# Performance work log

Measured on AMD Instinct MI355X. Metric: run time of the kernel, lower is better.

## Reference

```python
import jax, jax.numpy as jnp
import numpy as np

B, T, C, H = 32, 256, 512, 512
T_OUT = 8 * T  # fixed padded expanded length (max duration per token = 8)
ALPHA = 1.0
EPS = 1e-5


def _layer_norm(x, g, b):
    mu = jnp.mean(x, axis=-1, keepdims=True)
    var = jnp.mean(jnp.square(x - mu), axis=-1, keepdims=True)
    return (x - mu) * jax.lax.rsqrt(var + EPS) * g + b


def _conv1d_same(x, w, b):
    # x: [B,T,Cin], w: [3,Cin,Cout] -> [B,T,Cout]
    y = jax.lax.conv_general_dilated(x, w, window_strides=(1,), padding='SAME',
                                     dimension_numbers=('NWC', 'WIO', 'NWC'))
    return y + b


def setup_inputs() -> dict:
    key = jax.random.key(0)
    ks = jax.random.split(key, 8)
    s1 = 1.0 / np.sqrt(3 * C)
    s2 = 1.0 / np.sqrt(3 * H)
    return {
        'x': jax.random.normal(ks[0], (B, T, C), jnp.float32),
        'true_durations': jax.random.randint(ks[1], (B, T), 0, 8, jnp.int32),
        'W1': jax.random.normal(ks[2], (3, C, H), jnp.float32) * s1,
        'b1': jnp.zeros((H,), jnp.float32),
        'g1': jnp.ones((H,), jnp.float32),
        'beta1': jnp.zeros((H,), jnp.float32),
        'W2': jax.random.normal(ks[3], (3, H, H), jnp.float32) * s2,
        'b2': jnp.zeros((H,), jnp.float32),
        'g2': jnp.ones((H,), jnp.float32),
        'beta2': jnp.zeros((H,), jnp.float32),
        'Wl': jax.random.normal(ks[4], (H, 1), jnp.float32) * (1.0 / np.sqrt(H)),
        'bl': jnp.zeros((1,), jnp.float32),
    }


def _duration_predictor(x, W1, b1, g1, beta1, W2, b2, g2, beta2, Wl, bl):
    h = jax.nn.relu(_layer_norm(_conv1d_same(x, W1, b1), g1, beta1))
    h = jax.nn.relu(_layer_norm(_conv1d_same(h, W2, b2), g2, beta2))
    return (h @ Wl + bl)[..., 0]  # [B,T]


def _expand_by_durations(x, dur):
    # cumsum-based gather: output position t takes source token i where
    # csum[i-1] <= t < csum[i]; positions >= total length are zero-padded.
    csum = jnp.cumsum(dur, axis=-1)  # [B,T]
    pos = jnp.arange(T_OUT, dtype=csum.dtype)  # [T_OUT]
    idx = jax.vmap(lambda c: jnp.searchsorted(c, pos, side='right'))(csum)  # [B,T_OUT]
    valid = pos[None, :] < csum[:, -1:]
    idx = jnp.clip(idx, 0, dur.shape[1] - 1)
    out = jnp.take_along_axis(x, idx[..., None], axis=1)  # [B,T_OUT,C]
    return out * valid[..., None].astype(x.dtype)


def reference(x, true_durations, W1, b1, g1, beta1, W2, b2, g2, beta2, Wl, bl):
    log_lengths = _duration_predictor(x, W1, b1, g1, beta1, W2, b2, g2, beta2, Wl, bl) * ALPHA
    res = _expand_by_durations(x, true_durations)
    return res, log_lengths
```

## Files before the change

### kernel.cpp

```cpp
#include <hip/hip_runtime.h>
#include <hip/hip_bf16.h>

#define B_    32
#define T_    256
#define C_    512
#define H_    512
#define TOUT_ 2048
#define TP_   258
#define K_    1536
#define EPS_  1e-5f

typedef __attribute__((ext_vector_type(8))) short bf16x8;
typedef __attribute__((ext_vector_type(4))) float f32x4;

#define GLL16(g, l)                                                        \
  __builtin_amdgcn_global_load_lds(                                        \
      (const __attribute__((address_space(1))) void*)(g),                  \
      (__attribute__((address_space(3))) void*)(l), 16, 0, 0)

__device__ __forceinline__ void wt_convert_block(const float* __restrict__ W,
                                                 __hip_bfloat16* __restrict__ Wt,
                                                 int k0, int n0, int tid,
                                                 float* tile ) {
  const int tx = tid & 31;
  const int ty = tid >> 5;
#pragma unroll
  for (int i = 0; i < 4; ++i)
    tile[(ty * 4 + i) * 33 + tx] = W[(size_t)(k0 + ty * 4 + i) * H_ + n0 + tx];
  __syncthreads();
#pragma unroll
  for (int i = 0; i < 4; ++i)
    Wt[(size_t)(n0 + ty * 4 + i) * K_ + k0 + tx] =
        __float2bfloat16(tile[tx * 33 + ty * 4 + i]);
}

__device__ __forceinline__ void csum_block(const int* __restrict__ dur,
                                           int* __restrict__ csum,
                                           int b, int tid, int* wsum) {
  int v = dur[b * T_ + tid];
#pragma unroll
  for (int off = 1; off < 64; off <<= 1) {
    int u = __shfl_up(v, off);
    if ((tid & 63) >= off) v += u;
  }
  if ((tid & 63) == 63) wsum[tid >> 6] = v;
  __syncthreads();
  int base = 0;
#pragma unroll
  for (int j = 0; j < 4; ++j)
    if (j < (tid >> 6)) base += wsum[j];
  csum[b * T_ + tid] = v + base;
}

__device__ __forceinline__ void expand_copy_block(const float* __restrict__ X,
                                                  const int* __restrict__ csum,
                                                  float* __restrict__ res,
                                                  int u, int tid) {
  const int wave = (tid >> 6) & 3, lane = tid & 63;
#pragma unroll
  for (int k = 0; k < 4; ++k) {
    const int sr = u * 16 + wave * 4 + k;
    const int b = sr >> 8, t = sr & 255;
    const int* cb = csum + b * T_;
    const int c0 = t ? cb[t - 1] : 0;
    const int d  = cb[t] - c0;
    if (d == 0) continue;
    const float* src = X + (size_t)sr * C_;
    const float4 v0 = *(const float4*)(src + lane * 4);
    const float4 v1 = *(const float4*)(src + 256 + lane * 4);
    float* dst = res + ((size_t)b * TOUT_ + c0) * C_;
    for (int j = 0; j < d; ++j) {
      *(float4*)(dst + (size_t)j * C_ + lane * 4)       = v0;
      *(float4*)(dst + (size_t)j * C_ + 256 + lane * 4) = v1;
    }
  }
}

__device__ __forceinline__ void expand_zero_block(const int* __restrict__ csum,
                                                  float* __restrict__ res,
                                                  int z, int tid) {
  const int b  = z >> 6;
  const int t0 = (z & 63) << 5;
  const int total = csum[b * T_ + 255];
  const float4 z4 = make_float4(0.f, 0.f, 0.f, 0.f);
  const int half = (tid >> 7) & 1, c4 = tid & 127;
#pragma unroll
  for (int rr = half; rr < 32; rr += 2) {
    const int r = t0 + rr;
    if (r >= total)
      *(float4*)(res + ((size_t)b * TOUT_ + r) * C_ + c4 * 4) = z4;
  }
}

__global__ __launch_bounds__(256) void prep_kernel(const float* __restrict__ X,
                                                   const float* __restrict__ W1,
                                                   const int* __restrict__ dur,
                                                   __hip_bfloat16* __restrict__ xpad,
                                                   __hip_bfloat16* __restrict__ hpad,
                                                   __hip_bfloat16* __restrict__ Wt1,
                                                   int* __restrict__ csum) {
  __shared__ float tile[32 * 33];
  const int tid = threadIdx.x;
  if (blockIdx.x >= 4896) {
    csum_block(dur, csum, blockIdx.x - 4896, tid, (int*)tile);
    return;
  }
  if (blockIdx.x >= 4128) {
    const int id = blockIdx.x - 4128;
    wt_convert_block(W1, Wt1, (id % 48) * 32, (id / 48) * 32, tid, tile);
    return;
  }
  const int row = blockIdx.x * 2 + (tid >> 7);
  const int b = row / TP_;
  const int t = row - b * TP_;
  const int c = (tid & 127) * 4;
  __hip_bfloat16* dst = xpad + (size_t)row * C_ + c;
  if (t == 0 || t == TP_ - 1) {
    ushort4 zz = make_ushort4(0, 0, 0, 0);
    *(ushort4*)dst = zz;
    *(ushort4*)(hpad + (size_t)row * C_ + c) = zz;
    return;
  }
  const float4 v = *(const float4*)(X + (size_t)(b * T_ + t - 1) * C_ + c);
  union { __hip_bfloat16 h[4]; ushort4 u; } o;
  o.h[0] = __float2bfloat16(v.x);
  o.h[1] = __float2bfloat16(v.y);
  o.h[2] = __float2bfloat16(v.z);
  o.h[3] = __float2bfloat16(v.w);
  *(ushort4*)dst = o.u;
}

__global__ __launch_bounds__(512) void conv_expand_kernel(
    const __hip_bfloat16* __restrict__ Apad,
    const __hip_bfloat16* __restrict__ Wt,
    const float* __restrict__ bias,
    float* __restrict__ Y,
    const float* __restrict__ X,
    const int* __restrict__ csum,
    float* __restrict__ res,
    const float* __restrict__ W2,
    __hip_bfloat16* __restrict__ Wt2,
    int ex_base) {
  __shared__ __hip_bfloat16 smA[2][2][4096];
  __shared__ __hip_bfloat16 smB[2][2][4096];

  const int tid = threadIdx.x;

  if (blockIdx.x >= 896) {
    const int id = (blockIdx.x - 896) * 2 + (tid >> 8);
    float* tile = (float*)smA + (tid >> 8) * (32 * 33);
    wt_convert_block(W2, Wt2, (id % 48) * 32, (id / 48) * 32, tid & 255, tile);
    return;
  }
  if (blockIdx.x >= 256) {
    const int u = ex_base + (blockIdx.x - 256) * 2 + (tid >> 8);
    const int st = tid & 255;
    if (u < 512) expand_copy_block(X, csum, res, u, st);
    else         expand_zero_block(csum, res, u - 512, st);
    return;
  }

  const int lane = tid & 63;
  const int wid  = tid >> 6;
  const int cid  = blockIdx.x;
  const int n0 = (cid & 3) << 7;
  const int m0 = (cid >> 2) << 7;
  const int b  = m0 >> 8;
  const int t0 = m0 & 255;
  const int wm = (wid >> 2) << 6;
  const int wn = (wid & 3) << 5;

  const int rowS = tid >> 2;
  const int gsw  = ((tid & 3) + rowS) & 3;
  const __hip_bfloat16* arowA = Apad + (size_t)(b * TP_ + t0 + rowS) * C_ + (gsw << 3);
  const __hip_bfloat16* browB = Wt + (size_t)(n0 + rowS) * K_ + (gsw << 3);

  f32x4 acc[4][2] = {};

  auto stage = [&](int buf, int k0) {
    const int kw = k0 >> 9;
    const int c0 = k0 & 511;
    const __hip_bfloat16* a0 = arowA + kw * C_ + c0;
    GLL16(a0,           &smA[buf][0][tid << 3]);
    GLL16(a0 + 32,      &smA[buf][1][tid << 3]);
    GLL16(browB + k0,      &smB[buf][0][tid << 3]);
    GLL16(browB + k0 + 32, &smB[buf][1][tid << 3]);
  };

  auto compute = [&](int buf) {
    const int g   = lane >> 4;
    const int r15 = lane & 15;
    const int sa  = ((g - r15) & 3) << 3;
#pragma unroll
    for (int sl = 0; sl < 2; ++sl) {
      const __hip_bfloat16* As = smA[buf][sl];
      const __hip_bfloat16* Bs = smB[buf][sl];
      bf16x8 aF[4], bF[2];
#pragma unroll
      for (int i = 0; i < 4; ++i)
        aF[i] = *(const bf16x8*)(As + ((wm + (i << 4) + r15) << 5) + sa);
#pragma unroll
      for (int i = 0; i < 2; ++i)
        bF[i] = *(const bf16x8*)(Bs + ((wn + (i << 4) + r15) << 5) + sa);
#pragma unroll
      for (int mi = 0; mi < 4; ++mi)
#pragma unroll
        for (int ni = 0; ni < 2; ++ni)
          acc[mi][ni] = __builtin_amdgcn_mfma_f32_16x16x32_bf16(
              aF[mi], bF[ni], acc[mi][ni], 0, 0, 0);
    }
  };

  asm volatile("s_waitcnt vmcnt(0)" ::: "memory");
  stage(0, 0);
  stage(1, 64);

  for (int s = 0; s < 22; ++s) {
    asm volatile("s_waitcnt vmcnt(4)" ::: "memory");
    __builtin_amdgcn_sched_barrier(0);
    __builtin_amdgcn_s_barrier();
    compute(s & 1);
    asm volatile("s_waitcnt lgkmcnt(0)" ::: "memory");
    __builtin_amdgcn_s_barrier();
    stage(s & 1, (s + 2) << 6);
  }
  asm volatile("s_waitcnt vmcnt(4)" ::: "memory");
  __builtin_amdgcn_sched_barrier(0);
  __builtin_amdgcn_s_barrier();
  compute(0);
  asm volatile("s_waitcnt vmcnt(0)" ::: "memory");
  __builtin_amdgcn_sched_barrier(0);
  __builtin_amdgcn_s_barrier();
  compute(1);

  const int cn_base = n0 + wn + (lane & 15);
  const int rm_base = m0 + wm + ((lane >> 4) << 2);
#pragma unroll
  for (int ni = 0; ni < 2; ++ni) {
    const int cn = cn_base + (ni << 4);
    const float bb = bias[cn];
#pragma unroll
    for (int mi = 0; mi < 4; ++mi) {
#pragma unroll
      for (int rq = 0; rq < 4; ++rq) {
        const int rm = rm_base + (mi << 4) + rq;
        Y[(size_t)rm * H_ + cn] = acc[mi][ni][rq] + bb;
      }
    }
  }
}

__global__ __launch_bounds__(256) void ln_relu_pad_kernel(const float* __restrict__ in,
                                                          const float* __restrict__ g,
                                                          const float* __restrict__ beta,
                                                          __hip_bfloat16* __restrict__ outpad) {
  const int wave = threadIdx.x >> 6;
  const int lane = threadIdx.x & 63;
  const int row  = blockIdx.x * 4 + wave;
  const float* r = in + (size_t)row * H_;

  const float4 v0 = *(const float4*)(r + lane * 4);
  const float4 v1 = *(const float4*)(r + 256 + lane * 4);

  float s = v0.x + v0.y + v0.z + v0.w + v1.x + v1.y + v1.z + v1.w;
  float q = v0.x * v0.x + v0.y * v0.y + v0.z * v0.z + v0.w * v0.w +
            v1.x * v1.x + v1.y * v1.y + v1.z * v1.z + v1.w * v1.w;
#pragma unroll
  for (int off = 32; off; off >>= 1) {
    s += __shfl_xor(s, off);
    q += __shfl_xor(q, off);
  }
  const float mu  = s * (1.0f / 512.0f);
  const float var = q * (1.0f / 512.0f) - mu * mu;
  const float rs  = rsqrtf(var + EPS_);

  const float4 g0 = *(const float4*)(g + lane * 4);
  const float4 g1 = *(const float4*)(g + 256 + lane * 4);
  const float4 e0 = *(const float4*)(beta + lane * 4);
  const float4 e1 = *(const float4*)(beta + 256 + lane * 4);

  union { __hip_bfloat16 h[4]; ushort4 u; } o0, o1;
  o0.h[0] = __float2bfloat16(fmaxf(0.f, (v0.x - mu) * rs * g0.x + e0.x));
  o0.h[1] = __float2bfloat16(fmaxf(0.f, (v0.y - mu) * rs * g0.y + e0.y));
  o0.h[2] = __float2bfloat16(fmaxf(0.f, (v0.z - mu) * rs * g0.z + e0.z));
  o0.h[3] = __float2bfloat16(fmaxf(0.f, (v0.w - mu) * rs * g0.w + e0.w));
  o1.h[0] = __float2bfloat16(fmaxf(0.f, (v1.x - mu) * rs * g1.x + e1.x));
  o1.h[1] = __float2bfloat16(fmaxf(0.f, (v1.y - mu) * rs * g1.y + e1.y));
  o1.h[2] = __float2bfloat16(fmaxf(0.f, (v1.z - mu) * rs * g1.z + e1.z));
  o1.h[3] = __float2bfloat16(fmaxf(0.f, (v1.w - mu) * rs * g1.w + e1.w));

  const int bq = row >> 8, t = row & 255;
  __hip_bfloat16* w = outpad + (size_t)(bq * TP_ + t + 1) * H_;
  *(ushort4*)(w + lane * 4)       = o0.u;
  *(ushort4*)(w + 256 + lane * 4) = o1.u;
}

__global__ __launch_bounds__(256) void ln_relu_linear_kernel(const float* __restrict__ in,
                                                             const float* __restrict__ g,
                                                             const float* __restrict__ beta,
                                                             const float* __restrict__ Wl,
                                                             const float* __restrict__ bl,
                                                             float* __restrict__ out) {
  const int wave = threadIdx.x >> 6;
  const int lane = threadIdx.x & 63;
  const int row  = blockIdx.x * 4 + wave;
  const float* r = in + (size_t)row * H_;

  const float4 v0 = *(const float4*)(r + lane * 4);
  const float4 v1 = *(const float4*)(r + 256 + lane * 4);

  float s = v0.x + v0.y + v0.z + v0.w + v1.x + v1.y + v1.z + v1.w;
  float q = v0.x * v0.x + v0.y * v0.y + v0.z * v0.z + v0.w * v0.w +
            v1.x * v1.x + v1.y * v1.y + v1.z * v1.z + v1.w * v1.w;
#pragma unroll
  for (int off = 32; off; off >>= 1) {
    s += __shfl_xor(s, off);
    q += __shfl_xor(q, off);
  }
  const float mu  = s * (1.0f / 512.0f);
  const float var = q * (1.0f / 512.0f) - mu * mu;
  const float rs  = rsqrtf(var + EPS_);

  const float4 g0 = *(const float4*)(g + lane * 4);
  const float4 g1 = *(const float4*)(g + 256 + lane * 4);
  const float4 e0 = *(const float4*)(beta + lane * 4);
  const float4 e1 = *(const float4*)(beta + 256 + lane * 4);
  const float4 w0 = *(const float4*)(Wl + lane * 4);
  const float4 w1 = *(const float4*)(Wl + 256 + lane * 4);

  float sd = 0.f;
  sd += fmaxf(0.f, (v0.x - mu) * rs * g0.x + e0.x) * w0.x;
  sd += fmaxf(0.f, (v0.y - mu) * rs * g0.y + e0.y) * w0.y;
  sd += fmaxf(0.f, (v0.z - mu) * rs * g0.z + e0.z) * w0.z;
  sd += fmaxf(0.f, (v0.w - mu) * rs * g0.w + e0.w) * w0.w;
  sd += fmaxf(0.f, (v1.x - mu) * rs * g1.x + e1.x) * w1.x;
  sd += fmaxf(0.f, (v1.y - mu) * rs * g1.y + e1.y) * w1.y;
  sd += fmaxf(0.f, (v1.z - mu) * rs * g1.z + e1.z) * w1.z;
  sd += fmaxf(0.f, (v1.w - mu) * rs * g1.w + e1.w) * w1.w;
#pragma unroll
  for (int off = 32; off; off >>= 1) sd += __shfl_xor(sd, off);

  if (lane == 0) out[row] = sd + bl[0];
}

extern "C" void kernel_launch(void* const* d_in, const int* in_sizes, int n_in,
                              void* d_out, int out_size, void* d_ws, size_t ws_size,
                              hipStream_t stream) {
  const float* x     = (const float*)d_in[0];
  const int*   dur   = (const int*)d_in[1];
  const float* W1    = (const float*)d_in[2];
  const float* b1    = (const float*)d_in[3];
  const float* g1    = (const float*)d_in[4];
  const float* beta1 = (const float*)d_in[5];
  const float* W2    = (const float*)d_in[6];
  const float* b2    = (const float*)d_in[7];
  const float* g2    = (const float*)d_in[8];
  const float* beta2 = (const float*)d_in[9];
  const float* Wl    = (const float*)d_in[10];
  const float* bl    = (const float*)d_in[11];

  float* out = (float*)d_out;
  float* res    = out;
  float* loglen = out + (size_t)B_ * TOUT_ * C_;

  char* ws = (char*)d_ws;
  __hip_bfloat16* xpad = (__hip_bfloat16*)ws;
  __hip_bfloat16* hpad = xpad + (size_t)B_ * TP_ * C_;
  __hip_bfloat16* Wt1  = hpad + (size_t)B_ * TP_ * C_;
  __hip_bfloat16* Wt2  = Wt1 + (size_t)H_ * K_;
  float* tmp1 = (float*)(Wt2 + (size_t)H_ * K_);
  int*   csum = (int*)(tmp1 + (size_t)B_ * T_ * H_);

  prep_kernel<<<4928, 256, 0, stream>>>(x, W1, dur, xpad, hpad, Wt1, csum);

  conv_expand_kernel<<<1280, 512, 0, stream>>>(xpad, Wt1, b1, tmp1,
                                               x, csum, res, W2, Wt2, 0);
  ln_relu_pad_kernel<<<B_ * T_ / 4, 256, 0, stream>>>(tmp1, g1, beta1, hpad);

  conv_expand_kernel<<<896, 512, 0, stream>>>(hpad, Wt2, b2, tmp1,
                                              x, csum, res, nullptr, nullptr, 1280);
  ln_relu_linear_kernel<<<B_ * T_ / 4, 256, 0, stream>>>(tmp1, g2, beta2, Wl, bl, loglen);
}
```

Measured before the change: 82.60 us.

## Fuse LayerNorm, ReLU and output projection into full-width conv GEMM epilogue

Each conv GEMM block now computes a full 128x512 output tile, so the whole hidden row is held in registers. That lets it apply bias, LayerNorm (via cross-wave partial sums in LDS), ReLU, and either the bf16 padded write or the final linear dot product directly in the epilogue. This removes the fp32 intermediate buffer round trips and the two standalone LayerNorm kernel launches. The trade-off is that only 64 GEMM blocks remain, each doing four times more work with a large accumulator footprint under a 2-blocks-per-CU bound. That raises the risk of register spills and of the GEMM becoming a long critical path next to the expand blocks.

```diff
diff --git a/kernel.cpp b/kernel.cpp
--- a/kernel.cpp
+++ b/kernel.cpp
@@ -130,30 +130,36 @@
   *(ushort4*)dst = o.u;
 }
 
-__global__ __launch_bounds__(512) void conv_expand_kernel(
+template <int MODE>
+__global__ __launch_bounds__(512, 2) void conv_fused_kernel(
     const __hip_bfloat16* __restrict__ Apad,
     const __hip_bfloat16* __restrict__ Wt,
     const float* __restrict__ bias,
-    float* __restrict__ Y,
+    const float* __restrict__ gam,
+    const float* __restrict__ bet,
+    const float* __restrict__ Wl,
+    const float* __restrict__ bl,
+    __hip_bfloat16* __restrict__ hout,
+    float* __restrict__ lout,
     const float* __restrict__ X,
     const int* __restrict__ csum,
     float* __restrict__ res,
     const float* __restrict__ W2,
     __hip_bfloat16* __restrict__ Wt2,
     int ex_base) {
-  __shared__ __hip_bfloat16 smA[2][2][4096];
-  __shared__ __hip_bfloat16 smB[2][2][4096];
+  __shared__ __hip_bfloat16 smA[2][4096];
+  __shared__ __hip_bfloat16 smB[2][16384];
 
   const int tid = threadIdx.x;
 
-  if (blockIdx.x >= 896) {
-    const int id = (blockIdx.x - 896) * 2 + (tid >> 8);
-    float* tile = (float*)smA + (tid >> 8) * (32 * 33);
+  if (blockIdx.x >= 704) {
+    const int id = (blockIdx.x - 704) * 2 + (tid >> 8);
+    float* tile = (float*)&smB[0][0] + (tid >> 8) * (32 * 33);
     wt_convert_block(W2, Wt2, (id % 48) * 32, (id / 48) * 32, tid & 255, tile);
     return;
   }
-  if (blockIdx.x >= 256) {
-    const int u = ex_base + (blockIdx.x - 256) * 2 + (tid >> 8);
+  if (blockIdx.x >= 64) {
+    const int u = ex_base + (blockIdx.x - 64) * 2 + (tid >> 8);
     const int st = tid & 255;
     if (u < 512) expand_copy_block(X, csum, res, u, st);
     else         expand_zero_block(csum, res, u - 512, st);
@@ -162,69 +168,64 @@
 
   const int lane = tid & 63;
   const int wid  = tid >> 6;
-  const int cid  = blockIdx.x;
-  const int n0 = (cid & 3) << 7;
-  const int m0 = (cid >> 2) << 7;
+  const int m0 = blockIdx.x << 7;
   const int b  = m0 >> 8;
   const int t0 = m0 & 255;
-  const int wm = (wid >> 2) << 6;
-  const int wn = (wid & 3) << 5;
+  const int wgrp   = wid >> 2;
+  const int wslice = wid & 3;
+  const int wm  = wgrp << 6;
+  const int wnn = wslice << 7;
 
   const int rowS = tid >> 2;
   const int gsw  = ((tid & 3) + rowS) & 3;
   const __hip_bfloat16* arowA = Apad + (size_t)(b * TP_ + t0 + rowS) * C_ + (gsw << 3);
-  const __hip_bfloat16* browB = Wt + (size_t)(n0 + rowS) * K_ + (gsw << 3);
-
-  f32x4 acc[4][2] = {};
+  const __hip_bfloat16* browB = Wt + (size_t)rowS * K_ + (gsw << 3);
+
+  f32x4 acc[4][8] = {};
 
   auto stage = [&](int buf, int k0) {
     const int kw = k0 >> 9;
     const int c0 = k0 & 511;
-    const __hip_bfloat16* a0 = arowA + kw * C_ + c0;
-    GLL16(a0,           &smA[buf][0][tid << 3]);
-    GLL16(a0 + 32,      &smA[buf][1][tid << 3]);
-    GLL16(browB + k0,      &smB[buf][0][tid << 3]);
-    GLL16(browB + k0 + 32, &smB[buf][1][tid << 3]);
+    GLL16(arowA + kw * C_ + c0, &smA[buf][tid << 3]);
+#pragma unroll
+    for (int j = 0; j < 4; ++j)
+      GLL16(browB + (size_t)(j * 128) * K_ + k0,
+            &smB[buf][(tid << 3) + (j << 12)]);
   };
 
   auto compute = [&](int buf) {
     const int g   = lane >> 4;
     const int r15 = lane & 15;
     const int sa  = ((g - r15) & 3) << 3;
-#pragma unroll
-    for (int sl = 0; sl < 2; ++sl) {
-      const __hip_bfloat16* As = smA[buf][sl];
-      const __hip_bfloat16* Bs = smB[buf][sl];
-      bf16x8 aF[4], bF[2];
-#pragma unroll
-      for (int i = 0; i < 4; ++i)
-        aF[i] = *(const bf16x8*)(As + ((wm + (i << 4) + r15) << 5) + sa);
-#pragma unroll
-      for (int i = 0; i < 2; ++i)
-        bF[i] = *(const bf16x8*)(Bs + ((wn + (i << 4) + r15) << 5) + sa);
-#pragma unroll
-      for (int mi = 0; mi < 4; ++mi)
-#pragma unroll
-        for (int ni = 0; ni < 2; ++ni)
-          acc[mi][ni] = __builtin_amdgcn_mfma_f32_16x16x32_bf16(
-              aF[mi], bF[ni], acc[mi][ni], 0, 0, 0);
-    }
+    bf16x8 aF[4], bF[8];
+#pragma unroll
+    for (int i = 0; i < 4; ++i)
+      aF[i] = *(const bf16x8*)(&smA[buf][((wm + (i << 4) + r15) << 5) + sa]);
+#pragma unroll
+    for (int i = 0; i < 8; ++i)
+      bF[i] = *(const bf16x8*)(&smB[buf][((wnn + (i << 4) + r15) << 5) + sa]);
+#pragma unroll
+    for (int mi = 0; mi < 4; ++mi)
+#pragma unroll
+      for (int ni = 0; ni < 8; ++ni)
+        acc[mi][ni] = __builtin_amdgcn_mfma_f32_16x16x32_bf16(
+            aF[mi], bF[ni], acc[mi][ni], 0, 0, 0);
   };
 
   asm volatile("s_waitcnt vmcnt(0)" ::: "memory");
   stage(0, 0);
-  stage(1, 64);
-
-  for (int s = 0; s < 22; ++s) {
-    asm volatile("s_waitcnt vmcnt(4)" ::: "memory");
+  stage(1, 32);
+
+  for (int s = 0; s < 46; ++s) {
+    asm volatile("s_waitcnt vmcnt(5)" ::: "memory");
     __builtin_amdgcn_sched_barrier(0);
     __builtin_amdgcn_s_barrier();
     compute(s & 1);
     asm volatile("s_waitcnt lgkmcnt(0)" ::: "memory");
     __builtin_amdgcn_s_barrier();
-    stage(s & 1, (s + 2) << 6);
-  }
-  asm volatile("s_waitcnt vmcnt(4)" ::: "memory");
+    stage(s & 1, (s + 2) << 5);
+  }
+  asm volatile("s_waitcnt vmcnt(5)" ::: "memory");
   __builtin_amdgcn_sched_barrier(0);
   __builtin_amdgcn_s_barrier();
   compute(0);
@@ -233,114 +234,103 @@
   __builtin_amdgcn_s_barrier();
   compute(1);
 
-  const int cn_base = n0 + wn + (lane & 15);
-  const int rm_base = m0 + wm + ((lane >> 4) << 2);
-#pragma unroll
-  for (int ni = 0; ni < 2; ++ni) {
-    const int cn = cn_base + (ni << 4);
-    const float bb = bias[cn];
-#pragma unroll
-    for (int mi = 0; mi < 4; ++mi) {
-#pragma unroll
-      for (int rq = 0; rq < 4; ++rq) {
-        const int rm = rm_base + (mi << 4) + rq;
-        Y[(size_t)rm * H_ + cn] = acc[mi][ni][rq] + bb;
+  __syncthreads();
+  float* scr  = (float*)&smA[0][0];
+  float* scr2 = scr + 2048;
+
+  const int g   = lane >> 4;
+  const int r15 = lane & 15;
+
+  float bb8[8];
+#pragma unroll
+  for (int ni = 0; ni < 8; ++ni) bb8[ni] = bias[wnn + (ni << 4) + r15];
+
+#pragma unroll
+  for (int mi = 0; mi < 4; ++mi)
+#pragma unroll
+    for (int rq = 0; rq < 4; ++rq) {
+      float s = 0.f, q = 0.f;
+#pragma unroll
+      for (int ni = 0; ni < 8; ++ni) {
+        const float v = acc[mi][ni][rq] + bb8[ni];
+        s += v; q += v * v;
+      }
+#pragma unroll
+      for (int off = 1; off < 16; off <<= 1) {
+        s += __shfl_xor(s, off);
+        q += __shfl_xor(q, off);
+      }
+      if (r15 == 0) {
+        const int lrow = (mi << 4) + (g << 2) + rq;
+        const int base = (((wgrp << 6) + lrow) << 3) + (wslice << 1);
+        scr[base]     = s;
+        scr[base + 1] = q;
       }
     }
-  }
-}
-
-__global__ __launch_bounds__(256) void ln_relu_pad_kernel(const float* __restrict__ in,
-                                                          const float* __restrict__ g,
-                                                          const float* __restrict__ beta,
-                                                          __hip_bfloat16* __restrict__ outpad) {
-  const int wave = threadIdx.x >> 6;
-  const int lane = threadIdx.x & 63;
-  const int row  = blockIdx.x * 4 + wave;
-  const float* r = in + (size_t)row * H_;
-
-  const float4 v0 = *(const float4*)(r + lane * 4);
-  const float4 v1 = *(const float4*)(r + 256 + lane * 4);
-
-  float s = v0.x + v0.y + v0.z + v0.w + v1.x + v1.y + v1.z + v1.w;
-  float q = v0.x * v0.x + v0.y * v0.y + v0.z * v0.z + v0.w * v0.w +
-            v1.x * v1.x + v1.y * v1.y + v1.z * v1.z + v1.w * v1.w;
-#pragma unroll
-  for (int off = 32; off; off >>= 1) {
-    s += __shfl_xor(s, off);
-    q += __shfl_xor(q, off);
-  }
-  const float mu  = s * (1.0f / 512.0f);
-  const float var = q * (1.0f / 512.0f) - mu * mu;
-  const float rs  = rsqrtf(var + EPS_);
-
-  const float4 g0 = *(const float4*)(g + lane * 4);
-  const float4 g1 = *(const float4*)(g + 256 + lane * 4);
-  const float4 e0 = *(const float4*)(beta + lane * 4);
-  const float4 e1 = *(const float4*)(beta + 256 + lane * 4);
-
-  union { __hip_bfloat16 h[4]; ushort4 u; } o0, o1;
-  o0.h[0] = __float2bfloat16(fmaxf(0.f, (v0.x - mu) * rs * g0.x + e0.x));
-  o0.h[1] = __float2bfloat16(fmaxf(0.f, (v0.y - mu) * rs * g0.y + e0.y));
-  o0.h[2] = __float2bfloat16(fmaxf(0.f, (v0.z - mu) * rs * g0.z + e0.z));
-  o0.h[3] = __float2bfloat16(fmaxf(0.f, (v0.w - mu) * rs * g0.w + e0.w));
-  o1.h[0] = __float2bfloat16(fmaxf(0.f, (v1.x - mu) * rs * g1.x + e1.x));
-  o1.h[1] = __float2bfloat16(fmaxf(0.f, (v1.y - mu) * rs * g1.y + e1.y));
-  o1.h[2] = __float2bfloat16(fmaxf(0.f, (v1.z - mu) * rs * g1.z + e1.z));
-  o1.h[3] = __float2bfloat16(fmaxf(0.f, (v1.w - mu) * rs * g1.w + e1.w));
-
-  const int bq = row >> 8, t = row & 255;
-  __hip_bfloat16* w = outpad + (size_t)(bq * TP_ + t + 1) * H_;
-  *(ushort4*)(w + lane * 4)       = o0.u;
-  *(ushort4*)(w + 256 + lane * 4) = o1.u;
-}
-
-__global__ __launch_bounds__(256) void ln_relu_linear_kernel(const float* __restrict__ in,
-                                                             const float* __restrict__ g,
-                                                             const float* __restrict__ beta,
-                                                             const float* __restrict__ Wl,
-                                                             const float* __restrict__ bl,
-                                                             float* __restrict__ out) {
-  const int wave = threadIdx.x >> 6;
-  const int lane = threadIdx.x & 63;
-  const int row  = blockIdx.x * 4 + wave;
-  const float* r = in + (size_t)row * H_;
-
-  const float4 v0 = *(const float4*)(r + lane * 4);
-  const float4 v1 = *(const float4*)(r + 256 + lane * 4);
-
-  float s = v0.x + v0.y + v0.z + v0.w + v1.x + v1.y + v1.z + v1.w;
-  float q = v0.x * v0.x + v0.y * v0.y + v0.z * v0.z + v0.w * v0.w +
-            v1.x * v1.x + v1.y * v1.y + v1.z * v1.z + v1.w * v1.w;
-#pragma unroll
-  for (int off = 32; off; off >>= 1) {
-    s += __shfl_xor(s, off);
-    q += __shfl_xor(q, off);
-  }
-  const float mu  = s * (1.0f / 512.0f);
-  const float var = q * (1.0f / 512.0f) - mu * mu;
-  const float rs  = rsqrtf(var + EPS_);
-
-  const float4 g0 = *(const float4*)(g + lane * 4);
-  const float4 g1 = *(const float4*)(g + 256 + lane * 4);
-  const float4 e0 = *(const float4*)(beta + lane * 4);
-  const float4 e1 = *(const float4*)(beta + 256 + lane * 4);
-  const float4 w0 = *(const float4*)(Wl + lane * 4);
-  const float4 w1 = *(const float4*)(Wl + 256 + lane * 4);
-
-  float sd = 0.f;
-  sd += fmaxf(0.f, (v0.x - mu) * rs * g0.x + e0.x) * w0.x;
-  sd += fmaxf(0.f, (v0.y - mu) * rs * g0.y + e0.y) * w0.y;
-  sd += fmaxf(0.f, (v0.z - mu) * rs * g0.z + e0.z) * w0.z;
-  sd += fmaxf(0.f, (v0.w - mu) * rs * g0.w + e0.w) * w0.w;
-  sd += fmaxf(0.f, (v1.x - mu) * rs * g1.x + e1.x) * w1.x;
-  sd += fmaxf(0.f, (v1.y - mu) * rs * g1.y + e1.y) * w1.y;
-  sd += fmaxf(0.f, (v1.z - mu) * rs * g1.z + e1.z) * w1.z;
-  sd += fmaxf(0.f, (v1.w - mu) * rs * g1.w + e1.w) * w1.w;
-#pragma unroll
-  for (int off = 32; off; off >>= 1) sd += __shfl_xor(sd, off);
-
-  if (lane == 0) out[row] = sd + bl[0];
+  __syncthreads();
+
+  float g8[8], e8[8];
+#pragma unroll
+  for (int ni = 0; ni < 8; ++ni) {
+    g8[ni] = gam[wnn + (ni << 4) + r15];
+    e8[ni] = bet[wnn + (ni << 4) + r15];
+  }
+  float wl8[8];
+  if (MODE == 1) {
+#pragma unroll
+    for (int ni = 0; ni < 8; ++ni) wl8[ni] = Wl[wnn + (ni << 4) + r15];
+  }
+
+#pragma unroll
+  for (int mi = 0; mi < 4; ++mi)
+#pragma unroll
+    for (int rq = 0; rq < 4; ++rq) {
+      const int lrow = (mi << 4) + (g << 2) + rq;
+      const int base = ((wgrp << 6) + lrow) << 3;
+      const float S = scr[base] + scr[base + 2] + scr[base + 4] + scr[base + 6];
+      const float Q = scr[base + 1] + scr[base + 3] + scr[base + 5] + scr[base + 7];
+      const float mu  = S * (1.0f / 512.0f);
+      const float var = Q * (1.0f / 512.0f) - mu * mu;
+      const float rsv = rsqrtf(var + EPS_);
+      if (MODE == 0) {
+        __hip_bfloat16* wp =
+            hout + (size_t)(b * TP_ + t0 + (wgrp << 6) + lrow + 1) * C_;
+#pragma unroll
+        for (int ni = 0; ni < 8; ++ni) {
+          const float v = acc[mi][ni][rq] + bb8[ni];
+          const float o = fmaxf(0.f, (v - mu) * rsv * g8[ni] + e8[ni]);
+          wp[wnn + (ni << 4) + r15] = __float2bfloat16(o);
+        }
+      } else {
+        float sd = 0.f;
+#pragma unroll
+        for (int ni = 0; ni < 8; ++ni) {
+          const float v = acc[mi][ni][rq] + bb8[ni];
+          const float o = fmaxf(0.f, (v - mu) * rsv * g8[ni] + e8[ni]);
+          sd += o * wl8[ni];
+        }
+#pragma unroll
+        for (int off = 1; off < 16; off <<= 1) sd += __shfl_xor(sd, off);
+        if (r15 == 0)
+          scr2[(((wgrp << 6) + lrow) << 2) + wslice] = sd;
+      }
+    }
+
+  if (MODE == 1) {
+    __syncthreads();
+    if (wslice == 0 && r15 == 0) {
+#pragma unroll
+      for (int mi = 0; mi < 4; ++mi)
+#pragma unroll
+        for (int rq = 0; rq < 4; ++rq) {
+          const int lrow = (mi << 4) + (g << 2) + rq;
+          const int base2 = ((wgrp << 6) + lrow) << 2;
+          const float S = scr2[base2] + scr2[base2 + 1] +
+                          scr2[base2 + 2] + scr2[base2 + 3];
+          lout[m0 + (wgrp << 6) + lrow] = S + bl[0];
+        }
+    }
+  }
 }
 
 extern "C" void kernel_launch(void* const* d_in, const int* in_sizes, int n_in,
@@ -368,16 +358,15 @@
   __hip_bfloat16* hpad = xpad + (size_t)B_ * TP_ * C_;
   __hip_bfloat16* Wt1  = hpad + (size_t)B_ * TP_ * C_;
   __hip_bfloat16* Wt2  = Wt1 + (size_t)H_ * K_;
-  float* tmp1 = (float*)(Wt2 + (size_t)H_ * K_);
-  int*   csum = (int*)(tmp1 + (size_t)B_ * T_ * H_);
+  int*   csum = (int*)(Wt2 + (size_t)H_ * K_);
 
   prep_kernel<<<4928, 256, 0, stream>>>(x, W1, dur, xpad, hpad, Wt1, csum);
 
-  conv_expand_kernel<<<1280, 512, 0, stream>>>(xpad, Wt1, b1, tmp1,
-                                               x, csum, res, W2, Wt2, 0);
-  ln_relu_pad_kernel<<<B_ * T_ / 4, 256, 0, stream>>>(tmp1, g1, beta1, hpad);
-
-  conv_expand_kernel<<<896, 512, 0, stream>>>(hpad, Wt2, b2, tmp1,
-                                              x, csum, res, nullptr, nullptr, 1280);
-  ln_relu_linear_kernel<<<B_ * T_ / 4, 256, 0, stream>>>(tmp1, g2, beta2, Wl, bl, loglen);
-}
+  conv_fused_kernel<0><<<1088, 512, 0, stream>>>(
+      xpad, Wt1, b1, g1, beta1, nullptr, nullptr, hpad, nullptr,
+      x, csum, res, W2, Wt2, 0);
+
+  conv_fused_kernel<1><<<704, 512, 0, stream>>>(
+      hpad, Wt2, b2, g2, beta2, Wl, bl, nullptr, loglen,
+      x, csum, res, nullptr, nullptr, 1280);
+}
```

New measurement: 133.9 us. 62.1% more time.
